# Kernel tuning notes

Hardware: AMD Instinct MI355X
Metric: run time of the kernel (lower is better)

Reference implementation:

```python
import jax, jax.numpy as jnp
import numpy as np

N_NODES = 100000
N_EDGES = 3200000
C = 256
NEG_SLOPE = 0.2


def setup_inputs() -> dict:
    key = jax.random.key(0)
    k1, k2, k3, k4 = jax.random.split(key, 4)
    x = jax.random.normal(k1, (N_NODES, C), dtype=jnp.float32)
    # xavier_uniform on (2C, 1): bound = sqrt(6/(2C+1))
    bound = float(np.sqrt(6.0 / (2 * C + 1)))
    att = jax.random.uniform(k2, (2 * C, 1), dtype=jnp.float32, minval=-bound, maxval=bound)
    row = jax.random.randint(k3, (N_EDGES,), 0, N_NODES, dtype=jnp.int64)
    col = jax.random.randint(k4, (N_EDGES,), 0, N_NODES, dtype=jnp.int64)
    edge_index = jnp.stack([row, col], axis=0)
    return {"x": x, "att": att, "edge_index": edge_index}


def reference(x, att, edge_index):
    # Original: alpha = leaky_relu(cat([x[row], x[col]], -1) @ att)
    # Equivalent split form avoids materializing the [E, 2C] concat:
    # alpha_e = (x @ att[:C])[row] + (x @ att[C:])[col]
    row, col = edge_index[0], edge_index[1]
    n = x.shape[0]
    c = x.shape[1]
    s_src = (x @ att[:c]).squeeze(-1)  # (N,)
    s_dst = (x @ att[c:]).squeeze(-1)  # (N,)
    alpha = jax.nn.leaky_relu(s_src[row] + s_dst[col], negative_slope=NEG_SLOPE)  # (E,)
    # scatter_softmax over edges grouped by destination row id
    m = jax.ops.segment_max(alpha, row, num_segments=n)          # (N,)
    e = jnp.exp(alpha - m[row])                                   # (E,)
    denom = jax.ops.segment_sum(e, row, num_segments=n)          # (N,)
    out = e / denom[row]                                          # (E,)
    # torch code transposes [E,1] -> [1,E] before scatter_softmax; squeeze(-1) is a no-op
    return out[None, :]
```

## Files before the change

### kernel.cpp

```cpp
#include <hip/hip_runtime.h>

#define NN 100000
#define NE 3200000
#define CC 256
#define NEG_SLOPE 0.2f

#define SEG_S 32
#define SEG_P 8
#define PART_SZ 12500
#define SEG_BLOCK 1024
#define ESLICE (NE / SEG_S)

typedef __attribute__((ext_vector_type(8))) _Float16 half8;

__global__ __launch_bounds__(256) void node_scores_kernel(
    const float* __restrict__ x,
    const float* __restrict__ att,
    float* __restrict__ s_src,
    float* __restrict__ s_dst) {
  int gid  = blockIdx.x * blockDim.x + threadIdx.x;
  int node = gid >> 6;
  int lane = threadIdx.x & 63;
  if (node >= NN) return;
  const float4* xr = (const float4*)(x + (size_t)node * CC);
  const float4* a0 = (const float4*)att;
  const float4* a1 = (const float4*)(att + CC);
  float4 xv = xr[lane];
  float4 av = a0[lane];
  float4 bv = a1[lane];
  float s0 = xv.x * av.x + xv.y * av.y + xv.z * av.z + xv.w * av.w;
  float s1 = xv.x * bv.x + xv.y * bv.y + xv.z * bv.z + xv.w * bv.w;
#pragma unroll
  for (int off = 32; off > 0; off >>= 1) {
    s0 += __shfl_down(s0, off, 64);
    s1 += __shfl_down(s1, off, 64);
  }
  if (lane == 0) {
    s_src[node] = s0;
    s_dst[node] = s1;
  }
}

__global__ __launch_bounds__(256) void edge_exp_kernel(
    const int4* __restrict__ row4,
    const int4* __restrict__ col4,
    const float* __restrict__ s_src,
    const float* __restrict__ s_dst,
    half8* __restrict__ e_out) {
  int i = blockIdx.x * blockDim.x + threadIdx.x;
  if (i >= NE / 8) return;
  int4 ra = row4[2 * i], rb = row4[2 * i + 1];
  int4 ca = col4[2 * i], cb = col4[2 * i + 1];
  float a0 = s_src[ra.x] + s_dst[ca.x];
  float a1 = s_src[ra.y] + s_dst[ca.y];
  float a2 = s_src[ra.z] + s_dst[ca.z];
  float a3 = s_src[ra.w] + s_dst[ca.w];
  float a4 = s_src[rb.x] + s_dst[cb.x];
  float a5 = s_src[rb.y] + s_dst[cb.y];
  float a6 = s_src[rb.z] + s_dst[cb.z];
  float a7 = s_src[rb.w] + s_dst[cb.w];
  a0 = (a0 > 0.0f) ? a0 : NEG_SLOPE * a0;
  a1 = (a1 > 0.0f) ? a1 : NEG_SLOPE * a1;
  a2 = (a2 > 0.0f) ? a2 : NEG_SLOPE * a2;
  a3 = (a3 > 0.0f) ? a3 : NEG_SLOPE * a3;
  a4 = (a4 > 0.0f) ? a4 : NEG_SLOPE * a4;
  a5 = (a5 > 0.0f) ? a5 : NEG_SLOPE * a5;
  a6 = (a6 > 0.0f) ? a6 : NEG_SLOPE * a6;
  a7 = (a7 > 0.0f) ? a7 : NEG_SLOPE * a7;
  half8 h;
  h[0] = (_Float16)__expf(a0);
  h[1] = (_Float16)__expf(a1);
  h[2] = (_Float16)__expf(a2);
  h[3] = (_Float16)__expf(a3);
  h[4] = (_Float16)__expf(a4);
  h[5] = (_Float16)__expf(a5);
  h[6] = (_Float16)__expf(a6);
  h[7] = (_Float16)__expf(a7);
  e_out[i] = h;
}

__global__ __launch_bounds__(SEG_BLOCK) void segsum_kernel(
    const int* __restrict__ row,
    const _Float16* __restrict__ e,
    float* __restrict__ partial ) {
  __shared__ float lds[PART_SZ];
  int s = blockIdx.x;
  int p = blockIdx.y;
  for (int i = threadIdx.x; i < PART_SZ; i += SEG_BLOCK) lds[i] = 0.0f;
  __syncthreads();
  int lo = p * PART_SZ;
  const int4*  row4 = (const int4*)(row + s * ESLICE);
  const half8* e8   = (const half8*)(e + (size_t)s * ESLICE);
  const int n8 = ESLICE / 8;
  for (int i = threadIdx.x; i < n8; i += SEG_BLOCK) {
    int4 ra = row4[2 * i], rb = row4[2 * i + 1];
    half8 ev = e8[i];
    int r0 = ra.x - lo; if ((unsigned)r0 < PART_SZ) atomicAdd(&lds[r0], (float)ev[0]);
    int r1 = ra.y - lo; if ((unsigned)r1 < PART_SZ) atomicAdd(&lds[r1], (float)ev[1]);
    int r2 = ra.z - lo; if ((unsigned)r2 < PART_SZ) atomicAdd(&lds[r2], (float)ev[2]);
    int r3 = ra.w - lo; if ((unsigned)r3 < PART_SZ) atomicAdd(&lds[r3], (float)ev[3]);
    int r4 = rb.x - lo; if ((unsigned)r4 < PART_SZ) atomicAdd(&lds[r4], (float)ev[4]);
    int r5 = rb.y - lo; if ((unsigned)r5 < PART_SZ) atomicAdd(&lds[r5], (float)ev[5]);
    int r6 = rb.z - lo; if ((unsigned)r6 < PART_SZ) atomicAdd(&lds[r6], (float)ev[6]);
    int r7 = rb.w - lo; if ((unsigned)r7 < PART_SZ) atomicAdd(&lds[r7], (float)ev[7]);
  }
  __syncthreads();
  float* outp = partial + (size_t)s * NN + lo;
  for (int i = threadIdx.x; i < PART_SZ; i += SEG_BLOCK) outp[i] = lds[i];
}

__global__ __launch_bounds__(256) void reduce_kernel(
    const float* __restrict__ partial,
    float* __restrict__ denom) {
  int n4 = blockIdx.x * blockDim.x + threadIdx.x;
  if (n4 >= NN / 4) return;
  float4 sum = make_float4(0.f, 0.f, 0.f, 0.f);
#pragma unroll
  for (int s = 0; s < SEG_S; ++s) {
    float4 v = ((const float4*)(partial + (size_t)s * NN))[n4];
    sum.x += v.x; sum.y += v.y; sum.z += v.z; sum.w += v.w;
  }
  ((float4*)denom)[n4] = make_float4(1.f / sum.x, 1.f / sum.y, 1.f / sum.z, 1.f / sum.w);
}

__global__ __launch_bounds__(256) void edge_div_kernel(
    const int4* __restrict__ row4,
    const half8* __restrict__ e,
    const float* __restrict__ denom,
    float4* __restrict__ out4) {
  int i = blockIdx.x * blockDim.x + threadIdx.x;
  if (i >= NE / 8) return;
  int4 ra = row4[2 * i], rb = row4[2 * i + 1];
  half8 ev = e[i];
  float4 oa, ob;
  oa.x = (float)ev[0] * denom[ra.x];
  oa.y = (float)ev[1] * denom[ra.y];
  oa.z = (float)ev[2] * denom[ra.z];
  oa.w = (float)ev[3] * denom[ra.w];
  ob.x = (float)ev[4] * denom[rb.x];
  ob.y = (float)ev[5] * denom[rb.y];
  ob.z = (float)ev[6] * denom[rb.z];
  ob.w = (float)ev[7] * denom[rb.w];
  out4[2 * i]     = oa;
  out4[2 * i + 1] = ob;
}

extern "C" void kernel_launch(void* const* d_in, const int* in_sizes, int n_in,
                              void* d_out, int out_size, void* d_ws, size_t ws_size,
                              hipStream_t stream) {
  const float* x   = (const float*)d_in[0];
  const float* att = (const float*)d_in[1];
  const int* ei    = (const int*)d_in[2];
  const int* row   = ei;
  const int4* row4 = (const int4*)ei;
  const int4* col4 = (const int4*)(ei + NE);
  float4* out4     = (float4*)d_out;

  float* s_src      = (float*)d_ws;
  float* s_dst      = s_src + NN;
  float* denom      = s_dst + NN;
  _Float16* e_buf   = (_Float16*)(denom + NN);
  float* partial    = (float*)(e_buf + NE);

  node_scores_kernel<<<(NN * 64 + 255) / 256, 256, 0, stream>>>(x, att, s_src, s_dst);
  edge_exp_kernel<<<(NE / 8 + 255) / 256, 256, 0, stream>>>(
      row4, col4, s_src, s_dst, (half8*)e_buf);
  dim3 seg_grid(SEG_S, SEG_P);
  segsum_kernel<<<seg_grid, SEG_BLOCK, 0, stream>>>(row, e_buf, partial);
  reduce_kernel<<<(NN / 4 + 255) / 256, 256, 0, stream>>>(partial, denom);
  edge_div_kernel<<<(NE / 8 + 255) / 256, 256, 0, stream>>>(
      row4, (const half8*)e_buf, denom, out4);
}
```

Measured before the change: 235.4 us.

## Fuse all five GAT softmax stages into one persistent kernel with grid barriers

Replaces five separate kernel launches with a single persistent kernel of 256 blocks of 1024 threads. The stages are separated by software grid barriers built on atomic counters, and a memset resets the counters before each launch. The goal is to remove launch gaps and tail effects between stages. In exchange, it relies on all 256 blocks being co-resident to avoid deadlock, uses grid-stride loops with fewer threads in the streaming stages, and adds barrier spin overhead.

After: 531.8 us. 2.26x slower.

```diff
diff --git a/kernel.cpp b/kernel.cpp
--- a/kernel.cpp
+++ b/kernel.cpp
@@ -5,144 +5,160 @@
 #define CC 256
 #define NEG_SLOPE 0.2f
 
+#define NBLK 256
+#define NTHR 1024
+#define NTOT (NBLK * NTHR)
+#define NWAVES (NTOT / 64)
 #define SEG_S 32
 #define SEG_P 8
 #define PART_SZ 12500
-#define SEG_BLOCK 1024
 #define ESLICE (NE / SEG_S)
 
 typedef __attribute__((ext_vector_type(8))) _Float16 half8;
 
-__global__ __launch_bounds__(256) void node_scores_kernel(
+__device__ __forceinline__ void grid_barrier(unsigned* cnt, unsigned target) {
+  __syncthreads();
+  if (threadIdx.x == 0) {
+    __threadfence();
+    __hip_atomic_fetch_add(cnt, 1u, __ATOMIC_RELEASE, __HIP_MEMORY_SCOPE_AGENT);
+    while (__hip_atomic_load(cnt, __ATOMIC_ACQUIRE, __HIP_MEMORY_SCOPE_AGENT) < target) {
+      __builtin_amdgcn_s_sleep(2);
+    }
+    __threadfence();
+  }
+  __syncthreads();
+}
+
+__global__ __launch_bounds__(NTHR, 4) void gat_mono_kernel(
     const float* __restrict__ x,
     const float* __restrict__ att,
+    const int* __restrict__ row,
+    const int* __restrict__ col,
     float* __restrict__ s_src,
-    float* __restrict__ s_dst) {
-  int gid  = blockIdx.x * blockDim.x + threadIdx.x;
-  int node = gid >> 6;
-  int lane = threadIdx.x & 63;
-  if (node >= NN) return;
-  const float4* xr = (const float4*)(x + (size_t)node * CC);
-  const float4* a0 = (const float4*)att;
-  const float4* a1 = (const float4*)(att + CC);
-  float4 xv = xr[lane];
-  float4 av = a0[lane];
-  float4 bv = a1[lane];
-  float s0 = xv.x * av.x + xv.y * av.y + xv.z * av.z + xv.w * av.w;
-  float s1 = xv.x * bv.x + xv.y * bv.y + xv.z * bv.z + xv.w * bv.w;
+    float* __restrict__ s_dst,
+    float* __restrict__ rdenom,
+    _Float16* __restrict__ e_buf,
+    float* __restrict__ partial,
+    unsigned* __restrict__ barriers,
+    float4* __restrict__ out4) {
+  __shared__ float tile[PART_SZ];
+  const int tid  = threadIdx.x;
+  const int gtid = blockIdx.x * NTHR + tid;
+
+  {
+    int wave = gtid >> 6;
+    int lane = tid & 63;
+    float4 av = ((const float4*)att)[lane];
+    float4 bv = ((const float4*)(att + CC))[lane];
+    for (int node = wave; node < NN; node += NWAVES) {
+      float4 xv = ((const float4*)(x + (size_t)node * CC))[lane];
+      float s0 = xv.x * av.x + xv.y * av.y + xv.z * av.z + xv.w * av.w;
+      float s1 = xv.x * bv.x + xv.y * bv.y + xv.z * bv.z + xv.w * bv.w;
 #pragma unroll
-  for (int off = 32; off > 0; off >>= 1) {
-    s0 += __shfl_down(s0, off, 64);
-    s1 += __shfl_down(s1, off, 64);
+      for (int off = 32; off > 0; off >>= 1) {
+        s0 += __shfl_down(s0, off, 64);
+        s1 += __shfl_down(s1, off, 64);
+      }
+      if (lane == 0) { s_src[node] = s0; s_dst[node] = s1; }
+    }
   }
-  if (lane == 0) {
-    s_src[node] = s0;
-    s_dst[node] = s1;
+  grid_barrier(barriers + 0, NBLK);
+
+  {
+    const int4* row4 = (const int4*)row;
+    const int4* col4 = (const int4*)col;
+    for (int i = gtid; i < NE / 8; i += NTOT) {
+      int4 ra = row4[2 * i], rb = row4[2 * i + 1];
+      int4 ca = col4[2 * i], cb = col4[2 * i + 1];
+      float a0 = s_src[ra.x] + s_dst[ca.x];
+      float a1 = s_src[ra.y] + s_dst[ca.y];
+      float a2 = s_src[ra.z] + s_dst[ca.z];
+      float a3 = s_src[ra.w] + s_dst[ca.w];
+      float a4 = s_src[rb.x] + s_dst[cb.x];
+      float a5 = s_src[rb.y] + s_dst[cb.y];
+      float a6 = s_src[rb.z] + s_dst[cb.z];
+      float a7 = s_src[rb.w] + s_dst[cb.w];
+      a0 = (a0 > 0.0f) ? a0 : NEG_SLOPE * a0;
+      a1 = (a1 > 0.0f) ? a1 : NEG_SLOPE * a1;
+      a2 = (a2 > 0.0f) ? a2 : NEG_SLOPE * a2;
+      a3 = (a3 > 0.0f) ? a3 : NEG_SLOPE * a3;
+      a4 = (a4 > 0.0f) ? a4 : NEG_SLOPE * a4;
+      a5 = (a5 > 0.0f) ? a5 : NEG_SLOPE * a5;
+      a6 = (a6 > 0.0f) ? a6 : NEG_SLOPE * a6;
+      a7 = (a7 > 0.0f) ? a7 : NEG_SLOPE * a7;
+      half8 h;
+      h[0] = (_Float16)__expf(a0);
+      h[1] = (_Float16)__expf(a1);
+      h[2] = (_Float16)__expf(a2);
+      h[3] = (_Float16)__expf(a3);
+      h[4] = (_Float16)__expf(a4);
+      h[5] = (_Float16)__expf(a5);
+      h[6] = (_Float16)__expf(a6);
+      h[7] = (_Float16)__expf(a7);
+      ((half8*)e_buf)[i] = h;
+    }
   }
-}
+  grid_barrier(barriers + 1, NBLK);
 
-__global__ __launch_bounds__(256) void edge_exp_kernel(
-    const int4* __restrict__ row4,
-    const int4* __restrict__ col4,
-    const float* __restrict__ s_src,
-    const float* __restrict__ s_dst,
-    half8* __restrict__ e_out) {
-  int i = blockIdx.x * blockDim.x + threadIdx.x;
-  if (i >= NE / 8) return;
-  int4 ra = row4[2 * i], rb = row4[2 * i + 1];
-  int4 ca = col4[2 * i], cb = col4[2 * i + 1];
-  float a0 = s_src[ra.x] + s_dst[ca.x];
-  float a1 = s_src[ra.y] + s_dst[ca.y];
-  float a2 = s_src[ra.z] + s_dst[ca.z];
-  float a3 = s_src[ra.w] + s_dst[ca.w];
-  float a4 = s_src[rb.x] + s_dst[cb.x];
-  float a5 = s_src[rb.y] + s_dst[cb.y];
-  float a6 = s_src[rb.z] + s_dst[cb.z];
-  float a7 = s_src[rb.w] + s_dst[cb.w];
-  a0 = (a0 > 0.0f) ? a0 : NEG_SLOPE * a0;
-  a1 = (a1 > 0.0f) ? a1 : NEG_SLOPE * a1;
-  a2 = (a2 > 0.0f) ? a2 : NEG_SLOPE * a2;
-  a3 = (a3 > 0.0f) ? a3 : NEG_SLOPE * a3;
-  a4 = (a4 > 0.0f) ? a4 : NEG_SLOPE * a4;
-  a5 = (a5 > 0.0f) ? a5 : NEG_SLOPE * a5;
-  a6 = (a6 > 0.0f) ? a6 : NEG_SLOPE * a6;
-  a7 = (a7 > 0.0f) ? a7 : NEG_SLOPE * a7;
-  half8 h;
-  h[0] = (_Float16)__expf(a0);
-  h[1] = (_Float16)__expf(a1);
-  h[2] = (_Float16)__expf(a2);
-  h[3] = (_Float16)__expf(a3);
-  h[4] = (_Float16)__expf(a4);
-  h[5] = (_Float16)__expf(a5);
-  h[6] = (_Float16)__expf(a6);
-  h[7] = (_Float16)__expf(a7);
-  e_out[i] = h;
-}
+  {
+    int s = blockIdx.x & (SEG_S - 1);
+    int p = blockIdx.x >> 5;
+    for (int i = tid; i < PART_SZ; i += NTHR) tile[i] = 0.0f;
+    __syncthreads();
+    int lo = p * PART_SZ;
+    const int4*  row4s = (const int4*)(row + s * ESLICE);
+    const half8* e8    = (const half8*)(e_buf + (size_t)s * ESLICE);
+    for (int i = tid; i < ESLICE / 8; i += NTHR) {
+      int4 ra = row4s[2 * i], rb = row4s[2 * i + 1];
+      half8 ev = e8[i];
+      int r0 = ra.x - lo; if ((unsigned)r0 < PART_SZ) atomicAdd(&tile[r0], (float)ev[0]);
+      int r1 = ra.y - lo; if ((unsigned)r1 < PART_SZ) atomicAdd(&tile[r1], (float)ev[1]);
+      int r2 = ra.z - lo; if ((unsigned)r2 < PART_SZ) atomicAdd(&tile[r2], (float)ev[2]);
+      int r3 = ra.w - lo; if ((unsigned)r3 < PART_SZ) atomicAdd(&tile[r3], (float)ev[3]);
+      int r4 = rb.x - lo; if ((unsigned)r4 < PART_SZ) atomicAdd(&tile[r4], (float)ev[4]);
+      int r5 = rb.y - lo; if ((unsigned)r5 < PART_SZ) atomicAdd(&tile[r5], (float)ev[5]);
+      int r6 = rb.z - lo; if ((unsigned)r6 < PART_SZ) atomicAdd(&tile[r6], (float)ev[6]);
+      int r7 = rb.w - lo; if ((unsigned)r7 < PART_SZ) atomicAdd(&tile[r7], (float)ev[7]);
+    }
+    __syncthreads();
+    float* outp = partial + (size_t)s * NN + lo;
+    for (int i = tid; i < PART_SZ; i += NTHR) outp[i] = tile[i];
+  }
+  grid_barrier(barriers + 2, NBLK);
 
-__global__ __launch_bounds__(SEG_BLOCK) void segsum_kernel(
-    const int* __restrict__ row,
-    const _Float16* __restrict__ e,
-    float* __restrict__ partial ) {
-  __shared__ float lds[PART_SZ];
-  int s = blockIdx.x;
-  int p = blockIdx.y;
-  for (int i = threadIdx.x; i < PART_SZ; i += SEG_BLOCK) lds[i] = 0.0f;
-  __syncthreads();
-  int lo = p * PART_SZ;
-  const int4*  row4 = (const int4*)(row + s * ESLICE);
-  const half8* e8   = (const half8*)(e + (size_t)s * ESLICE);
-  const int n8 = ESLICE / 8;
-  for (int i = threadIdx.x; i < n8; i += SEG_BLOCK) {
-    int4 ra = row4[2 * i], rb = row4[2 * i + 1];
-    half8 ev = e8[i];
-    int r0 = ra.x - lo; if ((unsigned)r0 < PART_SZ) atomicAdd(&lds[r0], (float)ev[0]);
-    int r1 = ra.y - lo; if ((unsigned)r1 < PART_SZ) atomicAdd(&lds[r1], (float)ev[1]);
-    int r2 = ra.z - lo; if ((unsigned)r2 < PART_SZ) atomicAdd(&lds[r2], (float)ev[2]);
-    int r3 = ra.w - lo; if ((unsigned)r3 < PART_SZ) atomicAdd(&lds[r3], (float)ev[3]);
-    int r4 = rb.x - lo; if ((unsigned)r4 < PART_SZ) atomicAdd(&lds[r4], (float)ev[4]);
-    int r5 = rb.y - lo; if ((unsigned)r5 < PART_SZ) atomicAdd(&lds[r5], (float)ev[5]);
-    int r6 = rb.z - lo; if ((unsigned)r6 < PART_SZ) atomicAdd(&lds[r6], (float)ev[6]);
-    int r7 = rb.w - lo; if ((unsigned)r7 < PART_SZ) atomicAdd(&lds[r7], (float)ev[7]);
+  {
+    for (int n4 = gtid; n4 < NN / 4; n4 += NTOT) {
+      float4 sum = make_float4(0.f, 0.f, 0.f, 0.f);
+#pragma unroll
+      for (int s2 = 0; s2 < SEG_S; ++s2) {
+        float4 v = ((const float4*)(partial + (size_t)s2 * NN))[n4];
+        sum.x += v.x; sum.y += v.y; sum.z += v.z; sum.w += v.w;
+      }
+      ((float4*)rdenom)[n4] =
+          make_float4(1.f / sum.x, 1.f / sum.y, 1.f / sum.z, 1.f / sum.w);
+    }
   }
-  __syncthreads();
-  float* outp = partial + (size_t)s * NN + lo;
-  for (int i = threadIdx.x; i < PART_SZ; i += SEG_BLOCK) outp[i] = lds[i];
-}
+  grid_barrier(barriers + 3, NBLK);
 
-__global__ __launch_bounds__(256) void reduce_kernel(
-    const float* __restrict__ partial,
-    float* __restrict__ denom) {
-  int n4 = blockIdx.x * blockDim.x + threadIdx.x;
-  if (n4 >= NN / 4) return;
-  float4 sum = make_float4(0.f, 0.f, 0.f, 0.f);
-#pragma unroll
-  for (int s = 0; s < SEG_S; ++s) {
-    float4 v = ((const float4*)(partial + (size_t)s * NN))[n4];
-    sum.x += v.x; sum.y += v.y; sum.z += v.z; sum.w += v.w;
+  {
+    const int4*  row4 = (const int4*)row;
+    const half8* e8   = (const half8*)e_buf;
+    for (int i = gtid; i < NE / 8; i += NTOT) {
+      int4 ra = row4[2 * i], rb = row4[2 * i + 1];
+      half8 ev = e8[i];
+      float4 oa, ob;
+      oa.x = (float)ev[0] * rdenom[ra.x];
+      oa.y = (float)ev[1] * rdenom[ra.y];
+      oa.z = (float)ev[2] * rdenom[ra.z];
+      oa.w = (float)ev[3] * rdenom[ra.w];
+      ob.x = (float)ev[4] * rdenom[rb.x];
+      ob.y = (float)ev[5] * rdenom[rb.y];
+      ob.z = (float)ev[6] * rdenom[rb.z];
+      ob.w = (float)ev[7] * rdenom[rb.w];
+      out4[2 * i]     = oa;
+      out4[2 * i + 1] = ob;
+    }
   }
-  ((float4*)denom)[n4] = make_float4(1.f / sum.x, 1.f / sum.y, 1.f / sum.z, 1.f / sum.w);
-}
-
-__global__ __launch_bounds__(256) void edge_div_kernel(
-    const int4* __restrict__ row4,
-    const half8* __restrict__ e,
-    const float* __restrict__ denom,
-    float4* __restrict__ out4) {
-  int i = blockIdx.x * blockDim.x + threadIdx.x;
-  if (i >= NE / 8) return;
-  int4 ra = row4[2 * i], rb = row4[2 * i + 1];
-  half8 ev = e[i];
-  float4 oa, ob;
-  oa.x = (float)ev[0] * denom[ra.x];
-  oa.y = (float)ev[1] * denom[ra.y];
-  oa.z = (float)ev[2] * denom[ra.z];
-  oa.w = (float)ev[3] * denom[ra.w];
-  ob.x = (float)ev[4] * denom[rb.x];
-  ob.y = (float)ev[5] * denom[rb.y];
-  ob.z = (float)ev[6] * denom[rb.z];
-  ob.w = (float)ev[7] * denom[rb.w];
-  out4[2 * i]     = oa;
-  out4[2 * i + 1] = ob;
 }
 
 extern "C" void kernel_launch(void* const* d_in, const int* in_sizes, int n_in,
@@ -152,22 +168,17 @@
   const float* att = (const float*)d_in[1];
   const int* ei    = (const int*)d_in[2];
   const int* row   = ei;
-  const int4* row4 = (const int4*)ei;
-  const int4* col4 = (const int4*)(ei + NE);
+  const int* col   = ei + NE;
   float4* out4     = (float4*)d_out;
 
-  float* s_src      = (float*)d_ws;
-  float* s_dst      = s_src + NN;
-  float* denom      = s_dst + NN;
-  _Float16* e_buf   = (_Float16*)(denom + NN);
-  float* partial    = (float*)(e_buf + NE);
+  unsigned* barriers = (unsigned*)d_ws;
+  float* s_src       = (float*)d_ws + 64;
+  float* s_dst       = s_src + NN;
+  float* rdenom      = s_dst + NN;
+  float* partial     = rdenom + NN;
+  _Float16* e_buf    = (_Float16*)(partial + (size_t)SEG_S * NN);
 
-  node_scores_kernel<<<(NN * 64 + 255) / 256, 256, 0, stream>>>(x, att, s_src, s_dst);
-  edge_exp_kernel<<<(NE / 8 + 255) / 256, 256, 0, stream>>>(
-      row4, col4, s_src, s_dst, (half8*)e_buf);
-  dim3 seg_grid(SEG_S, SEG_P);
-  segsum_kernel<<<seg_grid, SEG_BLOCK, 0, stream>>>(row, e_buf, partial);
-  reduce_kernel<<<(NN / 4 + 255) / 256, 256, 0, stream>>>(partial, denom);
-  edge_div_kernel<<<(NE / 8 + 255) / 256, 256, 0, stream>>>(
-      row4, (const half8*)e_buf, denom, out4);
+  hipMemsetAsync(d_ws, 0, 64 * sizeof(unsigned), stream);
+  gat_mono_kernel<<<NBLK, NTHR, 0, stream>>>(
+      x, att, row, col, s_src, s_dst, rdenom, e_buf, partial, barriers, out4);
 }
```
